# Performance work log

Hardware: AMD Instinct MI355X
Metric: run time of the kernel (lower is better)

Reference implementation:

```python
import jax, jax.numpy as jnp
import numpy as np

B, N, D, H = 4, 1024, 512, 8
DH = D // H  # per-head dim for V and for each of the two Q/K halves
LAM = 0.5


def setup_inputs() -> dict:
    key = jax.random.key(0)
    ks = jax.random.split(key, 7)
    s = 0.02
    return {
        "x": jax.random.normal(ks[0], (B, N, D), dtype=jnp.float32),
        "Wq": jax.random.normal(ks[1], (D, 2 * D), dtype=jnp.float32) * s,
        "bq": jax.random.normal(ks[2], (2 * D,), dtype=jnp.float32) * s,
        "Wk": jax.random.normal(ks[3], (D, 2 * D), dtype=jnp.float32) * s,
        "bk": jax.random.normal(ks[4], (2 * D,), dtype=jnp.float32) * s,
        "Wv": jax.random.normal(ks[5], (D, D), dtype=jnp.float32) * s,
        "bv": jax.random.normal(ks[6], (D,), dtype=jnp.float32) * s,
    }


def reference(x, Wq, bq, Wk, bk, Wv, bv):
    b, n, d = x.shape
    q = (x @ Wq + bq).reshape(b, n, H, 2 * DH).transpose(0, 2, 1, 3)  # [B,H,N,2*DH]
    k = (x @ Wk + bk).reshape(b, n, H, 2 * DH).transpose(0, 2, 1, 3)
    v = (x @ Wv + bv).reshape(b, n, H, DH).transpose(0, 2, 1, 3)      # [B,H,N,DH]
    q1, q2 = q[..., :DH], q[..., DH:]
    k1, k2 = k[..., :DH], k[..., DH:]
    scale = 1.0 / jnp.sqrt(jnp.float32(DH))
    a1 = jax.nn.softmax(jnp.einsum("bhqd,bhkd->bhqk", q1, k1) * scale, axis=-1)
    a2 = jax.nn.softmax(jnp.einsum("bhqd,bhkd->bhqk", q2, k2) * scale, axis=-1)
    attn = a1 - LAM * a2                                              # [B,H,N,N]
    out = jnp.einsum("bhqk,bhkd->bhqd", attn, v)                      # [B,H,N,DH]
    return out.transpose(0, 2, 1, 3).reshape(b, n, d)
```

## Files before the change

kernel.cpp:

```cpp
#include <hip/hip_runtime.h>
#include <hip/hip_bf16.h>

typedef unsigned short u16;
typedef unsigned int u32;
typedef short s16x8 __attribute__((ext_vector_type(8)));
typedef float f32x4 __attribute__((ext_vector_type(4)));

__device__ inline u16 f2bf(float f) {
  union { float f; unsigned int u; } v; v.f = f;
  unsigned int r = v.u + 0x7fffu + ((v.u >> 16) & 1u);
  return (u16)(r >> 16);
}

__device__ __forceinline__ u32 cvt_pk_bf16(float lo, float hi) {
  u32 r;
  asm("v_cvt_pk_bf16_f32 %0, %1, %2" : "=v"(r) : "v"(lo), "v"(hi));
  return r;
}

__device__ __forceinline__ void g2lds16(const u16* g, u16* l) {
  __builtin_amdgcn_global_load_lds((const __attribute__((address_space(1))) void*)g,
                                   (__attribute__((address_space(3))) void*)l, 16, 0, 0);
}

__global__ __launch_bounds__(256) void cast_x_kernel(const float* __restrict__ x,
                                                     u16* __restrict__ xb) {
  int i = (blockIdx.x * 256 + threadIdx.x) * 8;
  float4 a = *(const float4*)(x + i);
  float4 b = *(const float4*)(x + i + 4);
  s16x8 o;
  o[0] = (short)f2bf(a.x); o[1] = (short)f2bf(a.y);
  o[2] = (short)f2bf(a.z); o[3] = (short)f2bf(a.w);
  o[4] = (short)f2bf(b.x); o[5] = (short)f2bf(b.y);
  o[6] = (short)f2bf(b.z); o[7] = (short)f2bf(b.w);
  *(s16x8*)(xb + i) = o;
}

__global__ __launch_bounds__(256) void transpose_cast_w_all(const float* __restrict__ Wq,
                                                            const float* __restrict__ Wk,
                                                            const float* __restrict__ Wv,
                                                            u16* __restrict__ wt) {
  __shared__ float tile[64][65];
  int jg = blockIdx.x * 64;
  const float* src; int C, j0;
  if (jg < 1024)      { src = Wq; C = 1024; j0 = jg; }
  else if (jg < 2048) { src = Wk; C = 1024; j0 = jg - 1024; }
  else                { src = Wv; C = 512;  j0 = jg - 2048; }
  int k0 = blockIdx.y * 64;
  int tx = threadIdx.x % 64, ty4 = threadIdx.x / 64;
#pragma unroll
  for (int p = 0; p < 16; ++p) {
    int r = p * 4 + ty4;
    tile[r][tx] = src[(size_t)(k0 + r) * C + j0 + tx];
  }
  __syncthreads();
#pragma unroll
  for (int p = 0; p < 16; ++p) {
    int r = p * 4 + ty4;
    wt[(size_t)(jg + r) * 512 + k0 + tx] = f2bf(tile[tx][r]);
  }
}

__global__ __launch_bounds__(256, 2) void gemm_qkv(const u16* __restrict__ xb, const u16* __restrict__ wt,
                                                   const float* __restrict__ bq, const float* __restrict__ bk,
                                                   const float* __restrict__ bv,
                                                   u16* __restrict__ qa, u16* __restrict__ ka,
                                                   u16* __restrict__ va) {
  __shared__ __align__(16) u16 As[128 * 64];
  __shared__ __align__(16) u16 Bs[128 * 64];
  int m0 = blockIdx.x * 128, j0 = blockIdx.y * 128;
  int tid = threadIdx.x;
  int w = tid >> 6, lane = tid & 63, quad = lane >> 4, l16 = lane & 15;
  int wr = (w >> 1) * 64, wc = (w & 1) * 64;

  int srow[4], scol[4], sbase[4];
#pragma unroll
  for (int it = 0; it < 4; ++it) {
    int s = it * 256 + tid;
    srow[it] = s >> 3;
    scol[it] = (s & 7) ^ ((s >> 3) & 7);
    sbase[it] = (s & ~63) * 8;
  }

  f32x4 acc[4][4];
#pragma unroll
  for (int i = 0; i < 4; ++i)
#pragma unroll
    for (int j = 0; j < 4; ++j)
#pragma unroll
      for (int r = 0; r < 4; ++r) acc[i][j][r] = 0.f;

  for (int kk = 0; kk < 8; ++kk) {
    int k0 = kk * 64;
    __syncthreads();
#pragma unroll
    for (int it = 0; it < 4; ++it) {
      g2lds16(xb + (size_t)(m0 + srow[it]) * 512 + k0 + scol[it] * 8, &As[sbase[it]]);
      g2lds16(wt + (size_t)(j0 + srow[it]) * 512 + k0 + scol[it] * 8, &Bs[sbase[it]]);
    }
    __syncthreads();
#pragma unroll
    for (int kb = 0; kb < 2; ++kb) {
      s16x8 af[4], bfr[4];
#pragma unroll
      for (int rb = 0; rb < 4; ++rb) {
        int row = wr + rb * 16 + l16;
        af[rb] = *(const s16x8*)(&As[row * 64 + (((kb * 4 + quad) ^ (row & 7)) * 8)]);
      }
#pragma unroll
      for (int cb = 0; cb < 4; ++cb) {
        int row = wc + cb * 16 + l16;
        bfr[cb] = *(const s16x8*)(&Bs[row * 64 + (((kb * 4 + quad) ^ (row & 7)) * 8)]);
      }
#pragma unroll
      for (int rb = 0; rb < 4; ++rb)
#pragma unroll
        for (int cb = 0; cb < 4; ++cb)
          acc[rb][cb] = __builtin_amdgcn_mfma_f32_16x16x32_bf16(af[rb], bfr[cb], acc[rb][cb], 0, 0, 0);
    }
  }

#pragma unroll
  for (int cb = 0; cb < 4; ++cb) {
    int j = j0 + wc + cb * 16 + l16;
    float bias = (j < 1024) ? bq[j] : (j < 2048) ? bk[j - 1024] : bv[j - 2048];
#pragma unroll
    for (int rb = 0; rb < 4; ++rb) {
#pragma unroll
      for (int r = 0; r < 4; ++r) {
        int m = m0 + wr + rb * 16 + quad * 4 + r;
        int bidx = m >> 10, n = m & 1023;
        u16 o = f2bf(acc[rb][cb][r] + bias);
        if (j < 1024) {
          int h = j >> 7, r2 = j & 127;
          qa[((size_t)((bidx * 8 + h) * 1024 + n)) * 128 + r2] = o;
        } else if (j < 2048) {
          int jj = j - 1024, h = jj >> 7, r2 = jj & 127;
          ka[((size_t)((bidx * 8 + h) * 1024 + n)) * 128 + r2] = o;
        } else {
          int jj = j - 2048, h = jj >> 6, d = jj & 63;
          va[((size_t)((bidx * 8 + h) * 64 + d)) * 1024 + n] = o;
        }
      }
    }
  }
}

__global__ __launch_bounds__(256, 2) void attn_kernel(const u16* __restrict__ qa, const u16* __restrict__ ka,
                                                      const u16* __restrict__ va, float* __restrict__ out) {
  __shared__ __align__(16) u16 Ks[2][64 * 128];
  __shared__ __align__(16) u16 Vs[3][64 * 64];
  __shared__ __align__(16) u16 Ps[2][64 * 72];
  int bh = blockIdx.x, b = bh >> 3, h = bh & 7;
  int q0 = blockIdx.y * 64;
  int tid = threadIdx.x, w = tid >> 6, lane = tid & 63, quad = lane >> 4, l16 = lane & 15;

  const u16* qrow = qa + (size_t)(bh * 1024 + q0 + w * 16 + l16) * 128;
  s16x8 qf[2][2];
  qf[0][0] = *(const s16x8*)(qrow + quad * 8);
  qf[0][1] = *(const s16x8*)(qrow + 32 + quad * 8);
  qf[1][0] = *(const s16x8*)(qrow + 64 + quad * 8);
  qf[1][1] = *(const s16x8*)(qrow + 96 + quad * 8);

  f32x4 O1[5], O2[5];
#pragma unroll
  for (int i = 0; i < 5; ++i)
#pragma unroll
    for (int r = 0; r < 4; ++r) { O1[i][r] = 0.f; O2[i][r] = 0.f; }

  s16x8 onesf;
#pragma unroll
  for (int i = 0; i < 8; ++i) onesf[i] = (l16 == 0) ? (short)0x3F80 : (short)0;

  int krow[4], kcol[4], kbse[4];
#pragma unroll
  for (int it = 0; it < 4; ++it) {
    int s = it * 256 + tid;
    krow[it] = s >> 4; kcol[it] = (s & 15) ^ ((s >> 4) & 7); kbse[it] = (s & ~63) * 8;
  }
  int vrow[2], vcol[2], vbse[2];
#pragma unroll
  for (int it = 0; it < 2; ++it) {
    int s = it * 256 + tid;
    vrow[it] = s >> 3; vcol[it] = (s & 7) ^ ((s >> 3) & 7); vbse[it] = (s & ~63) * 8;
  }
  const u16* kgbase = ka + (size_t)bh * 1024 * 128;
  const u16* vgbase = va + (size_t)bh * 64 * 1024;

  auto stageK = [&](int n0, u16* Kd) {
#pragma unroll
    for (int it = 0; it < 4; ++it)
      g2lds16(kgbase + (size_t)(n0 + krow[it]) * 128 + kcol[it] * 8, Kd + kbse[it]);
  };
  auto stageV = [&](int n0, u16* Vd) {
#pragma unroll
    for (int it = 0; it < 2; ++it)
      g2lds16(vgbase + (size_t)vrow[it] * 1024 + n0 + vcol[it] * 8, Vd + vbse[it]);
  };

  stageK(0, &Ks[0][0]);
  stageV(0, &Vs[0][0]);
  __syncthreads();

  int prow = (w * 16 + l16) * 72;
  s16x8 pf[2][2];
  int cv = 0;

  for (int kt = 0; kt < 16; ++kt) {
    int kc = kt & 1;
    int nv = (cv == 2) ? 0 : cv + 1;
    int pv = (cv == 0) ? 2 : cv - 1;
    if (kt < 15) { stageK((kt + 1) * 64, &Ks[kc ^ 1][0]); stageV((kt + 1) * 64, &Vs[nv][0]); }

    if (kt > 0) {
#pragma unroll
      for (int hh = 0; hh < 2; ++hh) {
        pf[hh][0] = *(const s16x8*)(&Ps[hh][prow + quad * 8]);
        pf[hh][1] = *(const s16x8*)(&Ps[hh][prow + 32 + quad * 8]);
      }
    }

    const u16* KsC = &Ks[kc][0];
    f32x4 sv[2][4];
#pragma unroll
    for (int hh = 0; hh < 2; ++hh)
#pragma unroll
      for (int nt = 0; nt < 4; ++nt) {
        f32x4 s; s[0] = s[1] = s[2] = s[3] = 0.f;
#pragma unroll
        for (int kb = 0; kb < 2; ++kb) {
          int row = nt * 16 + l16;
          s16x8 kf = *(const s16x8*)(&KsC[row * 128 + (((hh * 8 + kb * 4 + quad) ^ (row & 7)) * 8)]);
          s = __builtin_amdgcn_mfma_f32_16x16x32_bf16(kf, qf[hh][kb], s, 0, 0, 0);
        }
        sv[hh][nt] = s;
      }

    if (kt > 0) {
      const u16* VsP = &Vs[pv][0];
      s16x8 vf[4][2];
#pragma unroll
      for (int ct = 0; ct < 4; ++ct)
#pragma unroll
        for (int kb = 0; kb < 2; ++kb) {
          int row = ct * 16 + l16;
          vf[ct][kb] = *(const s16x8*)(&VsP[row * 64 + (((kb * 4 + quad) ^ (row & 7)) * 8)]);
        }
#pragma unroll
      for (int ct = 0; ct < 5; ++ct) {
        s16x8 b0 = (ct < 4) ? vf[ct][0] : onesf;
        s16x8 b1 = (ct < 4) ? vf[ct][1] : onesf;
        O1[ct] = __builtin_amdgcn_mfma_f32_16x16x32_bf16(pf[0][0], b0, O1[ct], 0, 0, 0);
        O1[ct] = __builtin_amdgcn_mfma_f32_16x16x32_bf16(pf[0][1], b1, O1[ct], 0, 0, 0);
        O2[ct] = __builtin_amdgcn_mfma_f32_16x16x32_bf16(pf[1][0], b0, O2[ct], 0, 0, 0);
        O2[ct] = __builtin_amdgcn_mfma_f32_16x16x32_bf16(pf[1][1], b1, O2[ct], 0, 0, 0);
      }
    }

#pragma unroll
    for (int hh = 0; hh < 2; ++hh)
#pragma unroll
      for (int nt = 0; nt < 4; ++nt) {
        float e0 = __builtin_exp2f(sv[hh][nt][0] * 0.18033688f);
        float e1 = __builtin_exp2f(sv[hh][nt][1] * 0.18033688f);
        float e2 = __builtin_exp2f(sv[hh][nt][2] * 0.18033688f);
        float e3 = __builtin_exp2f(sv[hh][nt][3] * 0.18033688f);
        uint2 pw; pw.x = cvt_pk_bf16(e0, e1); pw.y = cvt_pk_bf16(e2, e3);
        *(uint2*)(&Ps[hh][prow + nt * 16 + quad * 4]) = pw;
      }

    cv = nv;
    __syncthreads();
  }

  {
#pragma unroll
    for (int hh = 0; hh < 2; ++hh) {
      pf[hh][0] = *(const s16x8*)(&Ps[hh][prow + quad * 8]);
      pf[hh][1] = *(const s16x8*)(&Ps[hh][prow + 32 + quad * 8]);
    }
    const u16* VsP = &Vs[0][0];
    s16x8 vf[4][2];
#pragma unroll
    for (int ct = 0; ct < 4; ++ct)
#pragma unroll
      for (int kb = 0; kb < 2; ++kb) {
        int row = ct * 16 + l16;
        vf[ct][kb] = *(const s16x8*)(&VsP[row * 64 + (((kb * 4 + quad) ^ (row & 7)) * 8)]);
      }
#pragma unroll
    for (int ct = 0; ct < 5; ++ct) {
      s16x8 b0 = (ct < 4) ? vf[ct][0] : onesf;
      s16x8 b1 = (ct < 4) ? vf[ct][1] : onesf;
      O1[ct] = __builtin_amdgcn_mfma_f32_16x16x32_bf16(pf[0][0], b0, O1[ct], 0, 0, 0);
      O1[ct] = __builtin_amdgcn_mfma_f32_16x16x32_bf16(pf[0][1], b1, O1[ct], 0, 0, 0);
      O2[ct] = __builtin_amdgcn_mfma_f32_16x16x32_bf16(pf[1][0], b0, O2[ct], 0, 0, 0);
      O2[ct] = __builtin_amdgcn_mfma_f32_16x16x32_bf16(pf[1][1], b1, O2[ct], 0, 0, 0);
    }
  }

  float inv1[4], inv2[4];
#pragma unroll
  for (int r = 0; r < 4; ++r) {
    float l1 = __shfl(O1[4][r], lane & 48, 64);
    float l2 = __shfl(O2[4][r], lane & 48, 64);
    inv1[r] = 1.0f / l1;
    inv2[r] = 1.0f / l2;
  }
  int nb = q0 + w * 16 + quad * 4;
#pragma unroll
  for (int ct = 0; ct < 4; ++ct)
#pragma unroll
    for (int r = 0; r < 4; ++r) {
      float val = O1[ct][r] * inv1[r] - 0.5f * O2[ct][r] * inv2[r];
      out[(size_t)(b * 1024 + nb + r) * 512 + h * 64 + ct * 16 + l16] = val;
    }
}

extern "C" void kernel_launch(void* const* d_in, const int* in_sizes, int n_in,
                              void* d_out, int out_size, void* d_ws, size_t ws_size,
                              hipStream_t stream) {
  (void)in_sizes; (void)n_in; (void)out_size; (void)ws_size;
  const float* x  = (const float*)d_in[0];
  const float* Wq = (const float*)d_in[1];
  const float* bq = (const float*)d_in[2];
  const float* Wk = (const float*)d_in[3];
  const float* bk = (const float*)d_in[4];
  const float* Wv = (const float*)d_in[5];
  const float* bv = (const float*)d_in[6];
  float* out = (float*)d_out;

  char* ws = (char*)d_ws;
  u16* xb = (u16*)(ws);
  u16* wt = (u16*)(ws + 4194304);
  u16* qa = (u16*)(ws + 6815744);
  u16* ka = (u16*)(ws + 15204352);
  u16* va = (u16*)(ws + 23592960);

  cast_x_kernel<<<1024, 256, 0, stream>>>(x, xb);
  transpose_cast_w_all<<<dim3(40, 8), 256, 0, stream>>>(Wq, Wk, Wv, wt);
  gemm_qkv<<<dim3(32, 20), 256, 0, stream>>>(xb, wt, bq, bk, bv, qa, ka, va);
  attn_kernel<<<dim3(32, 16), 256, 0, stream>>>(qa, ka, va, out);
}
```

Before: 134.8 us.

## Double query tile per attention block to reuse staged K/V tiles

Each attention workgroup now handles 128 query rows instead of 64, with each wave computing two 16-row sub-tiles that share the K fragments and V tiles staged in LDS. This halves global K/V traffic and staging work per query row and moves the V fragment loads earlier in the iteration. The cost is more registers per wave (launch bounds drop to one block per SIMD pair), a larger P buffer in LDS, and half as many workgroups (256), which lowers occupancy and may leave CUs underused.

```diff
diff --git a/kernel.cpp b/kernel.cpp
--- a/kernel.cpp
+++ b/kernel.cpp
@@ -146,27 +146,32 @@
   }
 }
 
-__global__ __launch_bounds__(256, 2) void attn_kernel(const u16* __restrict__ qa, const u16* __restrict__ ka,
+__global__ __launch_bounds__(256, 1) void attn_kernel(const u16* __restrict__ qa, const u16* __restrict__ ka,
                                                       const u16* __restrict__ va, float* __restrict__ out) {
   __shared__ __align__(16) u16 Ks[2][64 * 128];
   __shared__ __align__(16) u16 Vs[3][64 * 64];
-  __shared__ __align__(16) u16 Ps[2][64 * 72];
+  __shared__ __align__(16) u16 Ps[2][128 * 72];
   int bh = blockIdx.x, b = bh >> 3, h = bh & 7;
-  int q0 = blockIdx.y * 64;
+  int q0 = blockIdx.y * 128;
   int tid = threadIdx.x, w = tid >> 6, lane = tid & 63, quad = lane >> 4, l16 = lane & 15;
 
-  const u16* qrow = qa + (size_t)(bh * 1024 + q0 + w * 16 + l16) * 128;
-  s16x8 qf[2][2];
-  qf[0][0] = *(const s16x8*)(qrow + quad * 8);
-  qf[0][1] = *(const s16x8*)(qrow + 32 + quad * 8);
-  qf[1][0] = *(const s16x8*)(qrow + 64 + quad * 8);
-  qf[1][1] = *(const s16x8*)(qrow + 96 + quad * 8);
-
-  f32x4 O1[5], O2[5];
-#pragma unroll
-  for (int i = 0; i < 5; ++i)
-#pragma unroll
-    for (int r = 0; r < 4; ++r) { O1[i][r] = 0.f; O2[i][r] = 0.f; }
+  s16x8 qf[2][2][2];
+#pragma unroll
+  for (int s = 0; s < 2; ++s) {
+    const u16* qrow = qa + (size_t)(bh * 1024 + q0 + w * 32 + s * 16 + l16) * 128;
+    qf[s][0][0] = *(const s16x8*)(qrow + quad * 8);
+    qf[s][0][1] = *(const s16x8*)(qrow + 32 + quad * 8);
+    qf[s][1][0] = *(const s16x8*)(qrow + 64 + quad * 8);
+    qf[s][1][1] = *(const s16x8*)(qrow + 96 + quad * 8);
+  }
+
+  f32x4 O1[2][5], O2[2][5];
+#pragma unroll
+  for (int s = 0; s < 2; ++s)
+#pragma unroll
+    for (int i = 0; i < 5; ++i)
+#pragma unroll
+      for (int r = 0; r < 4; ++r) { O1[s][i][r] = 0.f; O2[s][i][r] = 0.f; }
 
   s16x8 onesf;
 #pragma unroll
@@ -202,8 +207,8 @@
   stageV(0, &Vs[0][0]);
   __syncthreads();
 
-  int prow = (w * 16 + l16) * 72;
-  s16x8 pf[2][2];
+  int prow0 = (w * 32 + l16) * 72;
+  s16x8 pf[2][2][2];
   int cv = 0;
 
   for (int kt = 0; kt < 16; ++kt) {
@@ -212,62 +217,73 @@
     int pv = (cv == 0) ? 2 : cv - 1;
     if (kt < 15) { stageK((kt + 1) * 64, &Ks[kc ^ 1][0]); stageV((kt + 1) * 64, &Vs[nv][0]); }
 
+    s16x8 vf[4][2];
     if (kt > 0) {
 #pragma unroll
-      for (int hh = 0; hh < 2; ++hh) {
-        pf[hh][0] = *(const s16x8*)(&Ps[hh][prow + quad * 8]);
-        pf[hh][1] = *(const s16x8*)(&Ps[hh][prow + 32 + quad * 8]);
-      }
+      for (int s = 0; s < 2; ++s)
+#pragma unroll
+        for (int hh = 0; hh < 2; ++hh) {
+          pf[s][hh][0] = *(const s16x8*)(&Ps[hh][prow0 + s * (16 * 72) + quad * 8]);
+          pf[s][hh][1] = *(const s16x8*)(&Ps[hh][prow0 + s * (16 * 72) + 32 + quad * 8]);
+        }
+      const u16* VsP = &Vs[pv][0];
+#pragma unroll
+      for (int ct = 0; ct < 4; ++ct)
+#pragma unroll
+        for (int kb = 0; kb < 2; ++kb) {
+          int row = ct * 16 + l16;
+          vf[ct][kb] = *(const s16x8*)(&VsP[row * 64 + (((kb * 4 + quad) ^ (row & 7)) * 8)]);
+        }
     }
 
     const u16* KsC = &Ks[kc][0];
-    f32x4 sv[2][4];
+    f32x4 sv[2][2][4];
 #pragma unroll
     for (int hh = 0; hh < 2; ++hh)
 #pragma unroll
       for (int nt = 0; nt < 4; ++nt) {
-        f32x4 s; s[0] = s[1] = s[2] = s[3] = 0.f;
+        f32x4 a0, a1;
+#pragma unroll
+        for (int r = 0; r < 4; ++r) { a0[r] = 0.f; a1[r] = 0.f; }
 #pragma unroll
         for (int kb = 0; kb < 2; ++kb) {
           int row = nt * 16 + l16;
           s16x8 kf = *(const s16x8*)(&KsC[row * 128 + (((hh * 8 + kb * 4 + quad) ^ (row & 7)) * 8)]);
-          s = __builtin_amdgcn_mfma_f32_16x16x32_bf16(kf, qf[hh][kb], s, 0, 0, 0);
-        }
-        sv[hh][nt] = s;
+          a0 = __builtin_amdgcn_mfma_f32_16x16x32_bf16(kf, qf[0][hh][kb], a0, 0, 0, 0);
+          a1 = __builtin_amdgcn_mfma_f32_16x16x32_bf16(kf, qf[1][hh][kb], a1, 0, 0, 0);
+        }
+        sv[0][hh][nt] = a0;
+        sv[1][hh][nt] = a1;
       }
 
     if (kt > 0) {
-      const u16* VsP = &Vs[pv][0];
-      s16x8 vf[4][2];
-#pragma unroll
-      for (int ct = 0; ct < 4; ++ct)
-#pragma unroll
-        for (int kb = 0; kb < 2; ++kb) {
-          int row = ct * 16 + l16;
-          vf[ct][kb] = *(const s16x8*)(&VsP[row * 64 + (((kb * 4 + quad) ^ (row & 7)) * 8)]);
-        }
 #pragma unroll
       for (int ct = 0; ct < 5; ++ct) {
         s16x8 b0 = (ct < 4) ? vf[ct][0] : onesf;
         s16x8 b1 = (ct < 4) ? vf[ct][1] : onesf;
-        O1[ct] = __builtin_amdgcn_mfma_f32_16x16x32_bf16(pf[0][0], b0, O1[ct], 0, 0, 0);
-        O1[ct] = __builtin_amdgcn_mfma_f32_16x16x32_bf16(pf[0][1], b1, O1[ct], 0, 0, 0);
-        O2[ct] = __builtin_amdgcn_mfma_f32_16x16x32_bf16(pf[1][0], b0, O2[ct], 0, 0, 0);
-        O2[ct] = __builtin_amdgcn_mfma_f32_16x16x32_bf16(pf[1][1], b1, O2[ct], 0, 0, 0);
-      }
-    }
-
-#pragma unroll
-    for (int hh = 0; hh < 2; ++hh)
-#pragma unroll
-      for (int nt = 0; nt < 4; ++nt) {
-        float e0 = __builtin_exp2f(sv[hh][nt][0] * 0.18033688f);
-        float e1 = __builtin_exp2f(sv[hh][nt][1] * 0.18033688f);
-        float e2 = __builtin_exp2f(sv[hh][nt][2] * 0.18033688f);
-        float e3 = __builtin_exp2f(sv[hh][nt][3] * 0.18033688f);
-        uint2 pw; pw.x = cvt_pk_bf16(e0, e1); pw.y = cvt_pk_bf16(e2, e3);
-        *(uint2*)(&Ps[hh][prow + nt * 16 + quad * 4]) = pw;
-      }
+#pragma unroll
+        for (int s = 0; s < 2; ++s) {
+          O1[s][ct] = __builtin_amdgcn_mfma_f32_16x16x32_bf16(pf[s][0][0], b0, O1[s][ct], 0, 0, 0);
+          O1[s][ct] = __builtin_amdgcn_mfma_f32_16x16x32_bf16(pf[s][0][1], b1, O1[s][ct], 0, 0, 0);
+          O2[s][ct] = __builtin_amdgcn_mfma_f32_16x16x32_bf16(pf[s][1][0], b0, O2[s][ct], 0, 0, 0);
+          O2[s][ct] = __builtin_amdgcn_mfma_f32_16x16x32_bf16(pf[s][1][1], b1, O2[s][ct], 0, 0, 0);
+        }
+      }
+    }
+
+#pragma unroll
+    for (int s = 0; s < 2; ++s)
+#pragma unroll
+      for (int hh = 0; hh < 2; ++hh)
+#pragma unroll
+        for (int nt = 0; nt < 4; ++nt) {
+          float e0 = __builtin_exp2f(sv[s][hh][nt][0] * 0.18033688f);
+          float e1 = __builtin_exp2f(sv[s][hh][nt][1] * 0.18033688f);
+          float e2 = __builtin_exp2f(sv[s][hh][nt][2] * 0.18033688f);
+          float e3 = __builtin_exp2f(sv[s][hh][nt][3] * 0.18033688f);
+          uint2 pw; pw.x = cvt_pk_bf16(e0, e1); pw.y = cvt_pk_bf16(e2, e3);
+          *(uint2*)(&Ps[hh][prow0 + s * (16 * 72) + nt * 16 + quad * 4]) = pw;
+        }
 
     cv = nv;
     __syncthreads();
@@ -275,10 +291,12 @@
 
   {
 #pragma unroll
-    for (int hh = 0; hh < 2; ++hh) {
-      pf[hh][0] = *(const s16x8*)(&Ps[hh][prow + quad * 8]);
-      pf[hh][1] = *(const s16x8*)(&Ps[hh][prow + 32 + quad * 8]);
-    }
+    for (int s = 0; s < 2; ++s)
+#pragma unroll
+      for (int hh = 0; hh < 2; ++hh) {
+        pf[s][hh][0] = *(const s16x8*)(&Ps[hh][prow0 + s * (16 * 72) + quad * 8]);
+        pf[s][hh][1] = *(const s16x8*)(&Ps[hh][prow0 + s * (16 * 72) + 32 + quad * 8]);
+      }
     const u16* VsP = &Vs[0][0];
     s16x8 vf[4][2];
 #pragma unroll
@@ -292,29 +310,35 @@
     for (int ct = 0; ct < 5; ++ct) {
       s16x8 b0 = (ct < 4) ? vf[ct][0] : onesf;
       s16x8 b1 = (ct < 4) ? vf[ct][1] : onesf;
-      O1[ct] = __builtin_amdgcn_mfma_f32_16x16x32_bf16(pf[0][0], b0, O1[ct], 0, 0, 0);
-      O1[ct] = __builtin_amdgcn_mfma_f32_16x16x32_bf16(pf[0][1], b1, O1[ct], 0, 0, 0);
-      O2[ct] = __builtin_amdgcn_mfma_f32_16x16x32_bf16(pf[1][0], b0, O2[ct], 0, 0, 0);
-      O2[ct] = __builtin_amdgcn_mfma_f32_16x16x32_bf16(pf[1][1], b1, O2[ct], 0, 0, 0);
-    }
-  }
-
-  float inv1[4], inv2[4];
-#pragma unroll
-  for (int r = 0; r < 4; ++r) {
-    float l1 = __shfl(O1[4][r], lane & 48, 64);
-    float l2 = __shfl(O2[4][r], lane & 48, 64);
-    inv1[r] = 1.0f / l1;
-    inv2[r] = 1.0f / l2;
-  }
-  int nb = q0 + w * 16 + quad * 4;
-#pragma unroll
-  for (int ct = 0; ct < 4; ++ct)
+#pragma unroll
+      for (int s = 0; s < 2; ++s) {
+        O1[s][ct] = __builtin_amdgcn_mfma_f32_16x16x32_bf16(pf[s][0][0], b0, O1[s][ct], 0, 0, 0);
+        O1[s][ct] = __builtin_amdgcn_mfma_f32_16x16x32_bf16(pf[s][0][1], b1, O1[s][ct], 0, 0, 0);
+        O2[s][ct] = __builtin_amdgcn_mfma_f32_16x16x32_bf16(pf[s][1][0], b0, O2[s][ct], 0, 0, 0);
+        O2[s][ct] = __builtin_amdgcn_mfma_f32_16x16x32_bf16(pf[s][1][1], b1, O2[s][ct], 0, 0, 0);
+      }
+    }
+  }
+
+#pragma unroll
+  for (int s = 0; s < 2; ++s) {
+    float inv1[4], inv2[4];
 #pragma unroll
     for (int r = 0; r < 4; ++r) {
-      float val = O1[ct][r] * inv1[r] - 0.5f * O2[ct][r] * inv2[r];
-      out[(size_t)(b * 1024 + nb + r) * 512 + h * 64 + ct * 16 + l16] = val;
-    }
+      float l1 = __shfl(O1[s][4][r], lane & 48, 64);
+      float l2 = __shfl(O2[s][4][r], lane & 48, 64);
+      inv1[r] = 1.0f / l1;
+      inv2[r] = 1.0f / l2;
+    }
+    int nb = q0 + w * 32 + s * 16 + quad * 4;
+#pragma unroll
+    for (int ct = 0; ct < 4; ++ct)
+#pragma unroll
+      for (int r = 0; r < 4; ++r) {
+        float val = O1[s][ct][r] * inv1[r] - 0.5f * O2[s][ct][r] * inv2[r];
+        out[(size_t)(b * 1024 + nb + r) * 512 + h * 64 + ct * 16 + l16] = val;
+      }
+  }
 }
 
 extern "C" void kernel_launch(void* const* d_in, const int* in_sizes, int n_in,
@@ -340,5 +364,5 @@
   cast_x_kernel<<<1024, 256, 0, stream>>>(x, xb);
   transpose_cast_w_all<<<dim3(40, 8), 256, 0, stream>>>(Wq, Wk, Wv, wt);
   gemm_qkv<<<dim3(32, 20), 256, 0, stream>>>(xb, wt, bq, bk, bv, qa, ka, va);
-  attn_kernel<<<dim3(32, 16), 256, 0, stream>>>(qa, ka, va, out);
-}
+  attn_kernel<<<dim3(32, 8), 256, 0, stream>>>(qa, ka, va, out);
+}
```

Result: slower. 150.4 us (+11.5%).

## Keep softmax probabilities in registers and feed PV MFMA directly

Applied to the files above, without the earlier changes.

Removes the shared-memory P staging buffer. The exp'd score fragments from the QK MFMA output are packed straight into PV MFMA A-operands, with V read from LDS in a permuted order to match the register layout. The one-iteration software skew of PV behind QK and the triple-buffered V are dropped. This saves LDS writes and reads plus LDS capacity, but loses the overlap of PV with the next QK and adds more, smaller 8-byte V loads.

```diff
diff --git a/kernel.cpp b/kernel.cpp
--- a/kernel.cpp
+++ b/kernel.cpp
@@ -4,6 +4,7 @@
 typedef unsigned short u16;
 typedef unsigned int u32;
 typedef short s16x8 __attribute__((ext_vector_type(8)));
+typedef short s16x4 __attribute__((ext_vector_type(4)));
 typedef float f32x4 __attribute__((ext_vector_type(4)));
 
 __device__ inline u16 f2bf(float f) {
@@ -149,8 +150,7 @@
 __global__ __launch_bounds__(256, 2) void attn_kernel(const u16* __restrict__ qa, const u16* __restrict__ ka,
                                                       const u16* __restrict__ va, float* __restrict__ out) {
   __shared__ __align__(16) u16 Ks[2][64 * 128];
-  __shared__ __align__(16) u16 Vs[3][64 * 64];
-  __shared__ __align__(16) u16 Ps[2][64 * 72];
+  __shared__ __align__(16) u16 Vs[2][64 * 64];
   int bh = blockIdx.x, b = bh >> 3, h = bh & 7;
   int q0 = blockIdx.y * 64;
   int tid = threadIdx.x, w = tid >> 6, lane = tid & 63, quad = lane >> 4, l16 = lane & 15;
@@ -202,101 +202,73 @@
   stageV(0, &Vs[0][0]);
   __syncthreads();
 
-  int prow = (w * 16 + l16) * 72;
-  s16x8 pf[2][2];
-  int cv = 0;
-
   for (int kt = 0; kt < 16; ++kt) {
-    int kc = kt & 1;
-    int nv = (cv == 2) ? 0 : cv + 1;
-    int pv = (cv == 0) ? 2 : cv - 1;
-    if (kt < 15) { stageK((kt + 1) * 64, &Ks[kc ^ 1][0]); stageV((kt + 1) * 64, &Vs[nv][0]); }
-
-    if (kt > 0) {
-#pragma unroll
-      for (int hh = 0; hh < 2; ++hh) {
-        pf[hh][0] = *(const s16x8*)(&Ps[hh][prow + quad * 8]);
-        pf[hh][1] = *(const s16x8*)(&Ps[hh][prow + 32 + quad * 8]);
-      }
-    }
-
-    const u16* KsC = &Ks[kc][0];
+    int cur = kt & 1;
+    if (kt < 15) { stageK((kt + 1) * 64, &Ks[cur ^ 1][0]); stageV((kt + 1) * 64, &Vs[cur ^ 1][0]); }
+
+    const u16* KsC = &Ks[cur][0];
     f32x4 sv[2][4];
 #pragma unroll
     for (int hh = 0; hh < 2; ++hh)
 #pragma unroll
       for (int nt = 0; nt < 4; ++nt) {
-        f32x4 s; s[0] = s[1] = s[2] = s[3] = 0.f;
+        f32x4 a; a[0] = a[1] = a[2] = a[3] = 0.f;
 #pragma unroll
         for (int kb = 0; kb < 2; ++kb) {
           int row = nt * 16 + l16;
           s16x8 kf = *(const s16x8*)(&KsC[row * 128 + (((hh * 8 + kb * 4 + quad) ^ (row & 7)) * 8)]);
-          s = __builtin_amdgcn_mfma_f32_16x16x32_bf16(kf, qf[hh][kb], s, 0, 0, 0);
+          a = __builtin_amdgcn_mfma_f32_16x16x32_bf16(kf, qf[hh][kb], a, 0, 0, 0);
         }
-        sv[hh][nt] = s;
-      }
-
-    if (kt > 0) {
-      const u16* VsP = &Vs[pv][0];
-      s16x8 vf[4][2];
-#pragma unroll
-      for (int ct = 0; ct < 4; ++ct)
-#pragma unroll
-        for (int kb = 0; kb < 2; ++kb) {
-          int row = ct * 16 + l16;
-          vf[ct][kb] = *(const s16x8*)(&VsP[row * 64 + (((kb * 4 + quad) ^ (row & 7)) * 8)]);
+        sv[hh][nt] = a;
+      }
+
+    const u16* VsC = &Vs[cur][0];
+    s16x8 vB[4][2];
+#pragma unroll
+    for (int ct = 0; ct < 4; ++ct) {
+      int row = ct * 16 + l16, rx = row & 7;
+#pragma unroll
+      for (int hf = 0; hf < 2; ++hf) {
+        union { s16x4 hl[2]; s16x8 v; } u;
+#pragma unroll
+        for (int j = 0; j < 2; ++j) {
+          int nt = 2 * hf + j;
+          int lc = 2 * nt + (quad >> 1);
+          u.hl[j] = *(const s16x4*)(&VsC[row * 64 + (((lc ^ rx) << 3) + ((quad & 1) << 2))]);
         }
-#pragma unroll
-      for (int ct = 0; ct < 5; ++ct) {
-        s16x8 b0 = (ct < 4) ? vf[ct][0] : onesf;
-        s16x8 b1 = (ct < 4) ? vf[ct][1] : onesf;
-        O1[ct] = __builtin_amdgcn_mfma_f32_16x16x32_bf16(pf[0][0], b0, O1[ct], 0, 0, 0);
-        O1[ct] = __builtin_amdgcn_mfma_f32_16x16x32_bf16(pf[0][1], b1, O1[ct], 0, 0, 0);
-        O2[ct] = __builtin_amdgcn_mfma_f32_16x16x32_bf16(pf[1][0], b0, O2[ct], 0, 0, 0);
-        O2[ct] = __builtin_amdgcn_mfma_f32_16x16x32_bf16(pf[1][1], b1, O2[ct], 0, 0, 0);
-      }
-    }
-
+        vB[ct][hf] = u.v;
+      }
+    }
+
+    s16x8 pA[2][2];
 #pragma unroll
     for (int hh = 0; hh < 2; ++hh)
 #pragma unroll
-      for (int nt = 0; nt < 4; ++nt) {
-        float e0 = __builtin_exp2f(sv[hh][nt][0] * 0.18033688f);
-        float e1 = __builtin_exp2f(sv[hh][nt][1] * 0.18033688f);
-        float e2 = __builtin_exp2f(sv[hh][nt][2] * 0.18033688f);
-        float e3 = __builtin_exp2f(sv[hh][nt][3] * 0.18033688f);
-        uint2 pw; pw.x = cvt_pk_bf16(e0, e1); pw.y = cvt_pk_bf16(e2, e3);
-        *(uint2*)(&Ps[hh][prow + nt * 16 + quad * 4]) = pw;
-      }
-
-    cv = nv;
+      for (int hf = 0; hf < 2; ++hf) {
+        union { u32 wd[4]; s16x8 v; } u;
+#pragma unroll
+        for (int j = 0; j < 2; ++j) {
+          int nt = 2 * hf + j;
+          float e0 = __builtin_exp2f(sv[hh][nt][0] * 0.18033688f);
+          float e1 = __builtin_exp2f(sv[hh][nt][1] * 0.18033688f);
+          float e2 = __builtin_exp2f(sv[hh][nt][2] * 0.18033688f);
+          float e3 = __builtin_exp2f(sv[hh][nt][3] * 0.18033688f);
+          u.wd[2 * j]     = cvt_pk_bf16(e0, e1);
+          u.wd[2 * j + 1] = cvt_pk_bf16(e2, e3);
+        }
+        pA[hh][hf] = u.v;
+      }
+
+#pragma unroll
+    for (int ct = 0; ct < 5; ++ct)
+#pragma unroll
+      for (int hf = 0; hf < 2; ++hf) {
+        s16x8 bf = (ct < 4) ? vB[ct][hf] : onesf;
+        O1[ct] = __builtin_amdgcn_mfma_f32_16x16x32_bf16(pA[0][hf], bf, O1[ct], 0, 0, 0);
+        O2[ct] = __builtin_amdgcn_mfma_f32_16x16x32_bf16(pA[1][hf], bf, O2[ct], 0, 0, 0);
+      }
+
     __syncthreads();
-  }
-
-  {
-#pragma unroll
-    for (int hh = 0; hh < 2; ++hh) {
-      pf[hh][0] = *(const s16x8*)(&Ps[hh][prow + quad * 8]);
-      pf[hh][1] = *(const s16x8*)(&Ps[hh][prow + 32 + quad * 8]);
-    }
-    const u16* VsP = &Vs[0][0];
-    s16x8 vf[4][2];
-#pragma unroll
-    for (int ct = 0; ct < 4; ++ct)
-#pragma unroll
-      for (int kb = 0; kb < 2; ++kb) {
-        int row = ct * 16 + l16;
-        vf[ct][kb] = *(const s16x8*)(&VsP[row * 64 + (((kb * 4 + quad) ^ (row & 7)) * 8)]);
-      }
-#pragma unroll
-    for (int ct = 0; ct < 5; ++ct) {
-      s16x8 b0 = (ct < 4) ? vf[ct][0] : onesf;
-      s16x8 b1 = (ct < 4) ? vf[ct][1] : onesf;
-      O1[ct] = __builtin_amdgcn_mfma_f32_16x16x32_bf16(pf[0][0], b0, O1[ct], 0, 0, 0);
-      O1[ct] = __builtin_amdgcn_mfma_f32_16x16x32_bf16(pf[0][1], b1, O1[ct], 0, 0, 0);
-      O2[ct] = __builtin_amdgcn_mfma_f32_16x16x32_bf16(pf[1][0], b0, O2[ct], 0, 0, 0);
-      O2[ct] = __builtin_amdgcn_mfma_f32_16x16x32_bf16(pf[1][1], b1, O2[ct], 0, 0, 0);
-    }
   }
 
   float inv1[4], inv2[4];
```

After: 134.9 us. About the same (+0.0%).
